# Optimization experiments

Hardware: AMD Instinct MI355X
Metric: run time of the kernel (lower is better)

The kernel has to match this reference:

```python
import jax, jax.numpy as jnp
import numpy as np
import math

B, S, HID = 4, 2048, 2048
H, KV, D = 16, 4, 128  # heads, kv heads, head_dim; n_rep = H//KV = 4
THETA = 1000000.0


def setup_inputs() -> dict:
    key = jax.random.key(0)
    ks = jax.random.split(key, 6)
    x = jax.random.normal(ks[0], (B, S, HID), dtype=jnp.float32)
    # real RoPE tables (theta=1e6), shape [S, D]
    inv_freq = 1.0 / (THETA ** (jnp.arange(0, D, 2, dtype=jnp.float32) / D))
    t = jnp.arange(S, dtype=jnp.float32)
    freqs = jnp.outer(t, inv_freq)                      # [S, D/2]
    emb = jnp.concatenate([freqs, freqs], axis=-1)      # [S, D]
    cos, sin = jnp.cos(emb), jnp.sin(emb)
    scale = 0.02
    wq = jax.random.normal(ks[1], (H * D, HID), dtype=jnp.float32) * scale
    wk = jax.random.normal(ks[2], (KV * D, HID), dtype=jnp.float32) * scale
    wv = jax.random.normal(ks[3], (KV * D, HID), dtype=jnp.float32) * scale
    wo = jax.random.normal(ks[4], (HID, H * D), dtype=jnp.float32) * scale
    return {"x": x, "cos": cos, "sin": sin, "wq": wq, "wk": wk, "wv": wv, "wo": wo}


def _rotate_half(t):
    half = t.shape[-1] // 2
    return jnp.concatenate([-t[..., half:], t[..., :half]], axis=-1)


def reference(x, cos, sin, wq, wk, wv, wo):
    b, s, _ = x.shape
    rep = H // KV
    # QKV projections (torch Linear: y = x @ W^T)
    q = (x @ wq.T).reshape(b, s, H, D)
    k = (x @ wk.T).reshape(b, s, KV, D)
    v = (x @ wv.T).reshape(b, s, KV, D)
    # RoPE, cos/sin broadcast over batch and heads: [1, S, 1, D]
    c = cos[None, :s, None, :]
    si = sin[None, :s, None, :]
    q = q * c + _rotate_half(q) * si
    k = k * c + _rotate_half(k) * si
    # GQA without materializing repeated KV: group q heads as [KV, rep]
    qg = q.reshape(b, s, KV, rep, D)
    scale = 1.0 / math.sqrt(D)
    # flash path in source: SDPA with default is_causal=False -> full (non-causal) attention
    scores = jnp.einsum('bqkrd,bskd->bkrqs', qg, k) * scale  # [B, KV, rep, S, S]
    attn = jax.nn.softmax(scores, axis=-1)
    out = jnp.einsum('bkrqs,bskd->bqkrd', attn, v).reshape(b, s, H * D)
    return out @ wo.T
```

## Files before the change

kernel.cpp:

```cpp
#include <hip/hip_runtime.h>
#include <stdint.h>

#define BB 4
#define SS 2048
#define HIDW 2048
#define NH 16
#define NKV 4
#define DD 128

typedef unsigned short u16;
typedef unsigned long long u64;
typedef unsigned int uint;
typedef __attribute__((ext_vector_type(8))) short bf16x8;
typedef __attribute__((ext_vector_type(4))) float f32x4;
typedef __attribute__((ext_vector_type(2))) float f32x2;
typedef __attribute__((ext_vector_type(2))) __bf16 bf16x2;

__device__ __forceinline__ u16 f2bf1(float f) {
  __bf16 h = (__bf16)f;
  return __builtin_bit_cast(u16, h);
}

__device__ __forceinline__ float bf2f(u16 v) {
  return __uint_as_float((uint)v << 16);
}

__device__ __forceinline__ uint pkbf(float a, float b) {
  f32x2 v = {a, b};
  bf16x2 h = __builtin_convertvector(v, bf16x2);
  return __builtin_bit_cast(uint, h);
}

__device__ __forceinline__ void gld_lds16(const void* g, void* s) {
  __builtin_amdgcn_global_load_lds(
      (const __attribute__((address_space(1))) void*)g,
      (__attribute__((address_space(3))) void*)(unsigned)(uintptr_t)s,
      16, 0, 0);
}

__global__ __launch_bounds__(256) void cast_f32_bf16(const float* __restrict__ in,
                                                     u16* __restrict__ out, int n4) {
  int i = blockIdx.x * 256 + threadIdx.x;
  if (i < n4) {
    float4 f = ((const float4*)in)[i];
    uint2 o;
    o.x = pkbf(f.x, f.y);
    o.y = pkbf(f.z, f.w);
    ((uint2*)out)[i] = o;
  }
}

__global__ __launch_bounds__(256) void gemm_bt(const u16* __restrict__ A,
                                               const u16* __restrict__ Bt,
                                               float* __restrict__ C,
                                               int M, int N, int K) {
  __shared__ u16 As[128 * 32];
  __shared__ u16 Bs[128 * 32];
  const int tid = threadIdx.x;
  const int wave = tid >> 6, lane = tid & 63;
  const int lr = lane & 15, lq = lane >> 4;
  const int row0 = blockIdx.y * 128, col0 = blockIdx.x * 128;
  const int wm = (wave >> 1) * 64, wn = (wave & 1) * 64;

  const int trow = tid >> 2;
  const int tblk = (tid & 3) ^ (trow & 3);
  const u16* aSrc = A + (size_t)(row0 + trow) * K + tblk * 8;
  const u16* bSrc = Bt + (size_t)(col0 + trow) * K + tblk * 8;
  char* ldsA = (char*)As + wave * 1024;
  char* ldsB = (char*)Bs + wave * 1024;

  f32x4 acc[4][4] = {};
  const int aoff = (wm + lr) * 32 + ((lq ^ (lr & 3)) * 8);
  const int boff = (wn + lr) * 32 + ((lq ^ (lr & 3)) * 8);

  for (int k0 = 0; k0 < K; k0 += 32) {
    __syncthreads();
    gld_lds16(aSrc + k0, ldsA);
    gld_lds16(aSrc + (size_t)64 * K + k0, ldsA + 4096);
    gld_lds16(bSrc + k0, ldsB);
    gld_lds16(bSrc + (size_t)64 * K + k0, ldsB + 4096);
    __syncthreads();
    bf16x8 a[4], b[4];
#pragma unroll
    for (int i = 0; i < 4; i++) a[i] = *(const bf16x8*)(As + aoff + i * 512);
#pragma unroll
    for (int j = 0; j < 4; j++) b[j] = *(const bf16x8*)(Bs + boff + j * 512);
#pragma unroll
    for (int i = 0; i < 4; i++)
#pragma unroll
      for (int j = 0; j < 4; j++)
        acc[i][j] = __builtin_amdgcn_mfma_f32_16x16x32_bf16(a[i], b[j], acc[i][j], 0, 0, 0);
  }
#pragma unroll
  for (int i = 0; i < 4; i++) {
    int row = row0 + wm + i * 16 + lq * 4;
#pragma unroll
    for (int j = 0; j < 4; j++) {
      int col = col0 + wn + j * 16 + lr;
      float* cp = C + (size_t)row * N + col;
#pragma unroll
      for (int r = 0; r < 4; r++) cp[(size_t)r * N] = acc[i][j][r];
    }
  }
}

__global__ __launch_bounds__(256) void gemm_bt_bf16(const u16* __restrict__ A,
                                                    const u16* __restrict__ Bt,
                                                    u16* __restrict__ C,
                                                    int M, int N, int K) {
  __shared__ u16 As[128 * 32];
  __shared__ u16 Bs[128 * 32];
  const int tid = threadIdx.x;
  const int wave = tid >> 6, lane = tid & 63;
  const int lr = lane & 15, lq = lane >> 4;
  const int row0 = blockIdx.y * 128, col0 = blockIdx.x * 128;
  const int wm = (wave >> 1) * 64, wn = (wave & 1) * 64;

  const int trow = tid >> 2;
  const int tblk = (tid & 3) ^ (trow & 3);
  const u16* aSrc = A + (size_t)(row0 + trow) * K + tblk * 8;
  const u16* bSrc = Bt + (size_t)(col0 + trow) * K + tblk * 8;
  char* ldsA = (char*)As + wave * 1024;
  char* ldsB = (char*)Bs + wave * 1024;

  f32x4 acc[4][4] = {};
  const int aoff = (wm + lr) * 32 + ((lq ^ (lr & 3)) * 8);
  const int boff = (wn + lr) * 32 + ((lq ^ (lr & 3)) * 8);

  for (int k0 = 0; k0 < K; k0 += 32) {
    __syncthreads();
    gld_lds16(aSrc + k0, ldsA);
    gld_lds16(aSrc + (size_t)64 * K + k0, ldsA + 4096);
    gld_lds16(bSrc + k0, ldsB);
    gld_lds16(bSrc + (size_t)64 * K + k0, ldsB + 4096);
    __syncthreads();
    bf16x8 a[4], b[4];
#pragma unroll
    for (int i = 0; i < 4; i++) a[i] = *(const bf16x8*)(As + aoff + i * 512);
#pragma unroll
    for (int j = 0; j < 4; j++) b[j] = *(const bf16x8*)(Bs + boff + j * 512);
#pragma unroll
    for (int i = 0; i < 4; i++)
#pragma unroll
      for (int j = 0; j < 4; j++)
        acc[i][j] = __builtin_amdgcn_mfma_f32_16x16x32_bf16(a[i], b[j], acc[i][j], 0, 0, 0);
  }
#pragma unroll
  for (int i = 0; i < 4; i++) {
    int row = row0 + wm + i * 16 + lq * 4;
#pragma unroll
    for (int j = 0; j < 4; j++) {
      int col = col0 + wn + j * 16 + lr;
      u16* cp = C + (size_t)row * N + col;
#pragma unroll
      for (int r = 0; r < 4; r++) cp[(size_t)r * N] = f2bf1(acc[i][j][r]);
    }
  }
}

__global__ __launch_bounds__(256) void rope_qk(const u16* __restrict__ qkv,
                                               const float* __restrict__ cosT,
                                               const float* __restrict__ sinT,
                                               u16* __restrict__ qb, u16* __restrict__ kb) {
  const float qscale = 0.08838834764831845f;
  int tok = blockIdx.x;
  int b = tok >> 11, s = tok & (SS - 1);
  for (int p = threadIdx.x; p < (NH + NKV) * 64; p += 256) {
    int head = p >> 6, dd = p & 63;
    float c0 = cosT[s * DD + dd];
    float c1 = cosT[s * DD + dd + 64];
    float s0 = sinT[s * DD + dd];
    float s1 = sinT[s * DD + dd + 64];
    if (head < NH) {
      const u16* src = qkv + (size_t)tok * 3072 + head * DD;
      float x0 = bf2f(src[dd]), x1 = bf2f(src[dd + 64]);
      u16* dst = qb + ((size_t)(b * NH + head) * SS + s) * DD;
      dst[dd] = f2bf1((x0 * c0 - x1 * s0) * qscale);
      dst[dd + 64] = f2bf1((x1 * c1 + x0 * s1) * qscale);
    } else {
      int kv = head - NH;
      const u16* src = qkv + (size_t)tok * 3072 + 2048 + kv * DD;
      float x0 = bf2f(src[dd]), x1 = bf2f(src[dd + 64]);
      u16* dst = kb + ((size_t)(b * NKV + kv) * SS + s) * DD;
      dst[dd] = f2bf1(x0 * c0 - x1 * s0);
      dst[dd + 64] = f2bf1(x1 * c1 + x0 * s1);
    }
  }
}

__global__ __launch_bounds__(256) void v_trans(const u16* __restrict__ qkv,
                                               u16* __restrict__ vt) {
  __shared__ u16 tile[64][66];
  int bk = blockIdx.x;
  int b = bk >> 2, kv = bk & 3;
  int s0 = blockIdx.y * 64, d0 = blockIdx.z * 64;
  int t = threadIdx.x;
  int sl = t >> 2, dc = (t & 3) * 16;
  const u16* src = qkv + ((size_t)(b * SS + s0 + sl)) * 3072 + 2560 + kv * DD + d0 + dc;
  uint4 a0 = *(const uint4*)src;
  uint4 a1 = *(const uint4*)(src + 8);
  uint* lrow = (uint*)&tile[sl][dc];
  lrow[0] = a0.x; lrow[1] = a0.y; lrow[2] = a0.z; lrow[3] = a0.w;
  lrow[4] = a1.x; lrow[5] = a1.y; lrow[6] = a1.z; lrow[7] = a1.w;
  __syncthreads();
  int dl = t >> 2, sc = (t & 3) * 16;
  u16* dst = vt + ((size_t)bk * DD + d0 + dl) * SS + s0 + sc;
  uint4 o0, o1;
  o0.x = (uint)tile[sc + 0][dl] | ((uint)tile[sc + 1][dl] << 16);
  o0.y = (uint)tile[sc + 2][dl] | ((uint)tile[sc + 3][dl] << 16);
  o0.z = (uint)tile[sc + 4][dl] | ((uint)tile[sc + 5][dl] << 16);
  o0.w = (uint)tile[sc + 6][dl] | ((uint)tile[sc + 7][dl] << 16);
  o1.x = (uint)tile[sc + 8][dl] | ((uint)tile[sc + 9][dl] << 16);
  o1.y = (uint)tile[sc + 10][dl] | ((uint)tile[sc + 11][dl] << 16);
  o1.z = (uint)tile[sc + 12][dl] | ((uint)tile[sc + 13][dl] << 16);
  o1.w = (uint)tile[sc + 14][dl] | ((uint)tile[sc + 15][dl] << 16);
  *(uint4*)dst = o0;
  *(uint4*)(dst + 8) = o1;
}

__global__ __launch_bounds__(256, 2) void flash_attn(const u16* __restrict__ qb,
                                                     const u16* __restrict__ kb,
                                                     const u16* __restrict__ vt,
                                                     u16* __restrict__ ob) {
  __shared__ u16 Ks[2][64 * 128];
  __shared__ u16 Vs[2][128 * 64];
  __shared__ u16 Pt[128 * 64];
  const int tid = threadIdx.x;
  const int wave = tid >> 6, lane = tid & 63;
  const int lr = lane & 15, lq = lane >> 4;

  const int lin = blockIdx.y * 16 + blockIdx.x;
  const int xcd = lin & 7;
  const int slot = lin >> 3;
  const int pr = xcd + ((slot & 1) << 3);
  const int b = pr >> 2, kvh = pr & 3;
  const int rest = slot >> 1;
  const int h = kvh * 4 + (rest & 3);
  const int q0 = (rest >> 2) * 128;
  const int bh = b * 16 + h;

  const size_t kbase = (size_t)(b * NKV + kvh) * SS * DD;
  const size_t vbase = (size_t)(b * NKV + kvh) * DD * SS;

  bf16x8 qf[2][4];
#pragma unroll
  for (int nt = 0; nt < 2; nt++) {
    const u16* qrow = qb + ((size_t)bh * SS + q0 + wave * 32 + nt * 16 + lr) * DD + lq * 8;
#pragma unroll
    for (int kk = 0; kk < 4; kk++) qf[nt][kk] = *(const bf16x8*)(qrow + kk * 32);
  }

  f32x4 o_acc[8][2] = {};
  float l_i[2] = {0.0f, 0.0f};

  const int ktrow = tid >> 4;
  const int ktblk = (tid & 15) ^ ktrow;
  const u16* ksrc = kb + kbase + (size_t)ktrow * DD + ktblk * 8;
  const int vtrow = tid >> 3;
  const int vtblk = (tid & 7) ^ (vtrow & 7);
  const u16* vsrc = vt + vbase + (size_t)vtrow * SS + vtblk * 8;

  for (int s0 = 0; s0 < SS; s0 += 128) {
    __syncthreads();
#pragma unroll
    for (int hb = 0; hb < 2; hb++) {
      const u16* kS = ksrc + (size_t)(s0 + hb * 64) * DD;
      const u16* vS = vsrc + s0 + hb * 64;
      char* kd = (char*)(Ks[hb]) + wave * 1024;
      char* vd = (char*)(Vs[hb]) + wave * 1024;
#pragma unroll
      for (int c = 0; c < 4; c++) {
        gld_lds16(kS + (size_t)c * 16 * DD, kd + c * 4096);
        gld_lds16(vS + (size_t)c * 32 * SS, vd + c * 4096);
      }
    }
    __syncthreads();

#pragma unroll
    for (int hb = 0; hb < 2; hb++) {
      const u16* K = Ks[hb];
      const u16* V = Vs[hb];

      f32x4 sc[4][2] = {};
#pragma unroll
      for (int kk = 0; kk < 4; kk++) {
#pragma unroll
        for (int mt = 0; mt < 4; mt++) {
          bf16x8 kf = *(const bf16x8*)(K + (mt * 16 + lr) * 128 + (((kk * 4 + lq) ^ lr) * 8));
#pragma unroll
          for (int nt = 0; nt < 2; nt++)
            sc[mt][nt] = __builtin_amdgcn_mfma_f32_16x16x32_bf16(kf, qf[nt][kk], sc[mt][nt], 0, 0, 0);
        }
      }

#pragma unroll
      for (int nt = 0; nt < 2; nt++) {
        float rs = 0.0f;
#pragma unroll
        for (int mt = 0; mt < 4; mt++)
#pragma unroll
          for (int r = 0; r < 4; r++) {
            float p = __expf(sc[mt][nt][r]);
            sc[mt][nt][r] = p;
            rs += p;
          }
        l_i[nt] += rs;
        int prow = wave * 32 + nt * 16 + lr;
#pragma unroll
        for (int mt = 0; mt < 4; mt++) {
          u64 pw = (u64)pkbf(sc[mt][nt][0], sc[mt][nt][1]) |
                   ((u64)pkbf(sc[mt][nt][2], sc[mt][nt][3]) << 32);
          int bb = (mt * 2 + (lq >> 1)) ^ (lr & 7);
          *(u64*)((char*)Pt + prow * 128 + bb * 16 + (lq & 1) * 8) = pw;
        }
      }

#pragma unroll
      for (int kk2 = 0; kk2 < 2; kk2++) {
        bf16x8 pbf[2];
#pragma unroll
        for (int nt = 0; nt < 2; nt++) {
          int prow = wave * 32 + nt * 16 + lr;
          pbf[nt] = *(const bf16x8*)((char*)Pt + prow * 128 + (((kk2 * 4 + lq) ^ (lr & 7)) * 16));
        }
#pragma unroll
        for (int mt = 0; mt < 8; mt++) {
          bf16x8 vf = *(const bf16x8*)(V + (mt * 16 + lr) * 64 + (((kk2 * 4 + lq) ^ (lr & 7)) * 8));
#pragma unroll
          for (int nt = 0; nt < 2; nt++)
            o_acc[mt][nt] = __builtin_amdgcn_mfma_f32_16x16x32_bf16(vf, pbf[nt], o_acc[mt][nt], 0, 0, 0);
        }
      }
    }
  }

#pragma unroll
  for (int nt = 0; nt < 2; nt++) {
    float l = l_i[nt];
    l += __shfl_xor(l, 16, 64);
    l += __shfl_xor(l, 32, 64);
    float inv = 1.0f / l;
    size_t q = (size_t)q0 + wave * 32 + nt * 16 + lr;
    u16* dst = ob + ((size_t)b * SS + q) * HIDW + h * DD + lq * 4;
#pragma unroll
    for (int mt = 0; mt < 8; mt++) {
      uint2 pk;
      pk.x = pkbf(o_acc[mt][nt][0] * inv, o_acc[mt][nt][1] * inv);
      pk.y = pkbf(o_acc[mt][nt][2] * inv, o_acc[mt][nt][3] * inv);
      *(uint2*)(dst + mt * 16) = pk;
    }
  }
}

extern "C" void kernel_launch(void* const* d_in, const int* in_sizes, int n_in,
                              void* d_out, int out_size, void* d_ws, size_t ws_size,
                              hipStream_t stream) {
  const float* x = (const float*)d_in[0];
  const float* cosT = (const float*)d_in[1];
  const float* sinT = (const float*)d_in[2];
  const float* wq = (const float*)d_in[3];
  const float* wk = (const float*)d_in[4];
  const float* wv = (const float*)d_in[5];
  const float* wo = (const float*)d_in[6];
  float* out = (float*)d_out;

  char* ws = (char*)d_ws;
  size_t off = 0;
  auto alloc = [&](size_t bytes) {
    char* p = ws + off;
    off += (bytes + 255) & ~(size_t)255;
    return p;
  };
  const int M = BB * SS;
  u16* xb = (u16*)alloc((size_t)M * HIDW * 2);
  u16* wqkvb = (u16*)alloc((size_t)3072 * HIDW * 2);
  u16* wob = (u16*)alloc((size_t)HIDW * NH * DD * 2);
  u16* qkvb = (u16*)alloc((size_t)M * 3072 * 2);
  u16* qb = (u16*)alloc((size_t)BB * NH * SS * DD * 2);
  u16* kb = (u16*)alloc((size_t)BB * NKV * SS * DD * 2);
  u16* vt = (u16*)alloc((size_t)BB * NKV * DD * SS * 2);
  u16* ob = qkvb;

  cast_f32_bf16<<<(M * HIDW) / 1024, 256, 0, stream>>>(x, xb, (M * HIDW) / 4);
  cast_f32_bf16<<<(2048 * HIDW) / 1024, 256, 0, stream>>>(wq, wqkvb, (2048 * HIDW) / 4);
  cast_f32_bf16<<<(512 * HIDW) / 1024, 256, 0, stream>>>(wk, wqkvb + (size_t)2048 * HIDW,
                                                         (512 * HIDW) / 4);
  cast_f32_bf16<<<(512 * HIDW) / 1024, 256, 0, stream>>>(wv, wqkvb + (size_t)2560 * HIDW,
                                                         (512 * HIDW) / 4);
  cast_f32_bf16<<<(HIDW * NH * DD) / 1024, 256, 0, stream>>>(wo, wob, (HIDW * NH * DD) / 4);

  gemm_bt_bf16<<<dim3(3072 / 128, M / 128), 256, 0, stream>>>(xb, wqkvb, qkvb, M, 3072, HIDW);

  rope_qk<<<M, 256, 0, stream>>>(qkvb, cosT, sinT, qb, kb);
  v_trans<<<dim3(BB * NKV, SS / 64, DD / 64), 256, 0, stream>>>(qkvb, vt);

  flash_attn<<<dim3(SS / 128, BB * NH), 256, 0, stream>>>(qb, kb, vt, ob);

  gemm_bt<<<dim3(HIDW / 128, M / 128), 256, 0, stream>>>(ob, wob, out, M, HIDW, NH * DD);
}
```

Before: 554.3 us.

## Fuse RoPE and V transpose into QKV GEMM epilogue, merge weight casts

The QKV projection GEMM changes its warp tiling so each wave holds 32 rows by a full 128-column head. The epilogue can then apply RoPE and the q scale, or write V transposed, directly from the accumulators. This removes the intermediate qkv buffer round-trip and the separate rope_qk and v_trans kernels. The four weight cast launches are merged into one kernel. The cost is epilogue stores that are less coalesced, per-element cos/sin loads in the GEMM, and a different MFMA operand load pattern.

```diff
diff --git a/kernel.cpp b/kernel.cpp
--- a/kernel.cpp
+++ b/kernel.cpp
@@ -48,6 +48,32 @@
     o.y = pkbf(f.z, f.w);
     ((uint2*)out)[i] = o;
   }
+}
+
+__global__ __launch_bounds__(256) void cast_weights(const float* __restrict__ wq,
+                                                    const float* __restrict__ wk,
+                                                    const float* __restrict__ wv,
+                                                    const float* __restrict__ wo,
+                                                    u16* __restrict__ wqkvb,
+                                                    u16* __restrict__ wob) {
+  int i = blockIdx.x * 256 + threadIdx.x;
+  const float* src;
+  uint2* dst;
+  int off;
+  if (i < 1048576) {
+    src = wq; dst = (uint2*)wqkvb; off = i;
+  } else if (i < 1310720) {
+    src = wk; dst = (uint2*)(wqkvb + (size_t)2048 * 2048); off = i - 1048576;
+  } else if (i < 1572864) {
+    src = wv; dst = (uint2*)(wqkvb + (size_t)2560 * 2048); off = i - 1310720;
+  } else {
+    src = wo; dst = (uint2*)wob; off = i - 1572864;
+  }
+  float4 f = ((const float4*)src)[off];
+  uint2 o;
+  o.x = pkbf(f.x, f.y);
+  o.y = pkbf(f.z, f.w);
+  dst[off] = o;
 }
 
 __global__ __launch_bounds__(256) void gemm_bt(const u16* __restrict__ A,
@@ -104,17 +130,20 @@
   }
 }
 
-__global__ __launch_bounds__(256) void gemm_bt_bf16(const u16* __restrict__ A,
-                                                    const u16* __restrict__ Bt,
-                                                    u16* __restrict__ C,
-                                                    int M, int N, int K) {
+__global__ __launch_bounds__(256) void gemm_qkv_rope(const u16* __restrict__ A,
+                                                     const u16* __restrict__ Bt,
+                                                     const float* __restrict__ cosT,
+                                                     const float* __restrict__ sinT,
+                                                     u16* __restrict__ qb,
+                                                     u16* __restrict__ kb,
+                                                     u16* __restrict__ vt) {
   __shared__ u16 As[128 * 32];
   __shared__ u16 Bs[128 * 32];
   const int tid = threadIdx.x;
   const int wave = tid >> 6, lane = tid & 63;
   const int lr = lane & 15, lq = lane >> 4;
   const int row0 = blockIdx.y * 128, col0 = blockIdx.x * 128;
-  const int wm = (wave >> 1) * 64, wn = (wave & 1) * 64;
+  const int K = HIDW;
 
   const int trow = tid >> 2;
   const int tblk = (tid & 3) ^ (trow & 3);
@@ -123,9 +152,9 @@
   char* ldsA = (char*)As + wave * 1024;
   char* ldsB = (char*)Bs + wave * 1024;
 
-  f32x4 acc[4][4] = {};
-  const int aoff = (wm + lr) * 32 + ((lq ^ (lr & 3)) * 8);
-  const int boff = (wn + lr) * 32 + ((lq ^ (lr & 3)) * 8);
+  f32x4 acc[2][8] = {};
+  const int aoff = (wave * 32 + lr) * 32 + ((lq ^ (lr & 3)) * 8);
+  const int boff = lr * 32 + ((lq ^ (lr & 3)) * 8);
 
   for (int k0 = 0; k0 < K; k0 += 32) {
     __syncthreads();
@@ -134,88 +163,59 @@
     gld_lds16(bSrc + k0, ldsB);
     gld_lds16(bSrc + (size_t)64 * K + k0, ldsB + 4096);
     __syncthreads();
-    bf16x8 a[4], b[4];
-#pragma unroll
-    for (int i = 0; i < 4; i++) a[i] = *(const bf16x8*)(As + aoff + i * 512);
-#pragma unroll
-    for (int j = 0; j < 4; j++) b[j] = *(const bf16x8*)(Bs + boff + j * 512);
-#pragma unroll
-    for (int i = 0; i < 4; i++)
-#pragma unroll
-      for (int j = 0; j < 4; j++)
+    bf16x8 a[2], b[8];
+#pragma unroll
+    for (int i = 0; i < 2; i++) a[i] = *(const bf16x8*)(As + aoff + i * 512);
+#pragma unroll
+    for (int j = 0; j < 8; j++) b[j] = *(const bf16x8*)(Bs + boff + j * 512);
+#pragma unroll
+    for (int i = 0; i < 2; i++)
+#pragma unroll
+      for (int j = 0; j < 8; j++)
         acc[i][j] = __builtin_amdgcn_mfma_f32_16x16x32_bf16(a[i], b[j], acc[i][j], 0, 0, 0);
   }
-#pragma unroll
-  for (int i = 0; i < 4; i++) {
-    int row = row0 + wm + i * 16 + lq * 4;
-#pragma unroll
-    for (int j = 0; j < 4; j++) {
-      int col = col0 + wn + j * 16 + lr;
-      u16* cp = C + (size_t)row * N + col;
-#pragma unroll
-      for (int r = 0; r < 4; r++) cp[(size_t)r * N] = f2bf1(acc[i][j][r]);
-    }
-  }
-}
-
-__global__ __launch_bounds__(256) void rope_qk(const u16* __restrict__ qkv,
-                                               const float* __restrict__ cosT,
-                                               const float* __restrict__ sinT,
-                                               u16* __restrict__ qb, u16* __restrict__ kb) {
-  const float qscale = 0.08838834764831845f;
-  int tok = blockIdx.x;
-  int b = tok >> 11, s = tok & (SS - 1);
-  for (int p = threadIdx.x; p < (NH + NKV) * 64; p += 256) {
-    int head = p >> 6, dd = p & 63;
-    float c0 = cosT[s * DD + dd];
-    float c1 = cosT[s * DD + dd + 64];
-    float s0 = sinT[s * DD + dd];
-    float s1 = sinT[s * DD + dd + 64];
-    if (head < NH) {
-      const u16* src = qkv + (size_t)tok * 3072 + head * DD;
-      float x0 = bf2f(src[dd]), x1 = bf2f(src[dd + 64]);
-      u16* dst = qb + ((size_t)(b * NH + head) * SS + s) * DD;
-      dst[dd] = f2bf1((x0 * c0 - x1 * s0) * qscale);
-      dst[dd + 64] = f2bf1((x1 * c1 + x0 * s1) * qscale);
-    } else {
-      int kv = head - NH;
-      const u16* src = qkv + (size_t)tok * 3072 + 2048 + kv * DD;
-      float x0 = bf2f(src[dd]), x1 = bf2f(src[dd + 64]);
-      u16* dst = kb + ((size_t)(b * NKV + kv) * SS + s) * DD;
-      dst[dd] = f2bf1(x0 * c0 - x1 * s0);
-      dst[dd + 64] = f2bf1(x1 * c1 + x0 * s1);
-    }
-  }
-}
-
-__global__ __launch_bounds__(256) void v_trans(const u16* __restrict__ qkv,
-                                               u16* __restrict__ vt) {
-  __shared__ u16 tile[64][66];
-  int bk = blockIdx.x;
-  int b = bk >> 2, kv = bk & 3;
-  int s0 = blockIdx.y * 64, d0 = blockIdx.z * 64;
-  int t = threadIdx.x;
-  int sl = t >> 2, dc = (t & 3) * 16;
-  const u16* src = qkv + ((size_t)(b * SS + s0 + sl)) * 3072 + 2560 + kv * DD + d0 + dc;
-  uint4 a0 = *(const uint4*)src;
-  uint4 a1 = *(const uint4*)(src + 8);
-  uint* lrow = (uint*)&tile[sl][dc];
-  lrow[0] = a0.x; lrow[1] = a0.y; lrow[2] = a0.z; lrow[3] = a0.w;
-  lrow[4] = a1.x; lrow[5] = a1.y; lrow[6] = a1.z; lrow[7] = a1.w;
-  __syncthreads();
-  int dl = t >> 2, sc = (t & 3) * 16;
-  u16* dst = vt + ((size_t)bk * DD + d0 + dl) * SS + s0 + sc;
-  uint4 o0, o1;
-  o0.x = (uint)tile[sc + 0][dl] | ((uint)tile[sc + 1][dl] << 16);
-  o0.y = (uint)tile[sc + 2][dl] | ((uint)tile[sc + 3][dl] << 16);
-  o0.z = (uint)tile[sc + 4][dl] | ((uint)tile[sc + 5][dl] << 16);
-  o0.w = (uint)tile[sc + 6][dl] | ((uint)tile[sc + 7][dl] << 16);
-  o1.x = (uint)tile[sc + 8][dl] | ((uint)tile[sc + 9][dl] << 16);
-  o1.y = (uint)tile[sc + 10][dl] | ((uint)tile[sc + 11][dl] << 16);
-  o1.z = (uint)tile[sc + 12][dl] | ((uint)tile[sc + 13][dl] << 16);
-  o1.w = (uint)tile[sc + 14][dl] | ((uint)tile[sc + 15][dl] << 16);
-  *(uint4*)dst = o0;
-  *(uint4*)(dst + 8) = o1;
+
+  const int b_ = row0 >> 11;
+  const int s_base = (row0 & (SS - 1)) + wave * 32;
+  const int hsel = col0 >> 7;
+
+  if (hsel < 20) {
+    const float scale = (hsel < 16) ? 0.08838834764831845f : 1.0f;
+    u16* base = (hsel < 16)
+                    ? qb + (size_t)(b_ * NH + hsel) * SS * DD
+                    : kb + (size_t)(b_ * NKV + (hsel - 16)) * SS * DD;
+#pragma unroll
+    for (int i = 0; i < 2; i++) {
+#pragma unroll
+      for (int r = 0; r < 4; r++) {
+        int s = s_base + i * 16 + lq * 4 + r;
+        const float* cp = cosT + (size_t)s * DD;
+        const float* sp = sinT + (size_t)s * DD;
+        u16* drow = base + (size_t)s * DD;
+#pragma unroll
+        for (int j = 0; j < 4; j++) {
+          int d = j * 16 + lr;
+          float c = cp[d], si = sp[d];
+          float x0 = acc[i][j][r] * scale, x1 = acc[i][j + 4][r] * scale;
+          drow[d] = f2bf1(x0 * c - x1 * si);
+          drow[d + 64] = f2bf1(x1 * c + x0 * si);
+        }
+      }
+    }
+  } else {
+    const int kv = hsel - 20;
+#pragma unroll
+    for (int i = 0; i < 2; i++) {
+      int s = s_base + i * 16 + lq * 4;
+#pragma unroll
+      for (int j = 0; j < 8; j++) {
+        int d = j * 16 + lr;
+        u64 pw = (u64)pkbf(acc[i][j][0], acc[i][j][1]) |
+                 ((u64)pkbf(acc[i][j][2], acc[i][j][3]) << 32);
+        *(u64*)(vt + (size_t)((b_ * NKV + kv) * DD + d) * SS + s) = pw;
+      }
+    }
+  }
 }
 
 __global__ __launch_bounds__(256, 2) void flash_attn(const u16* __restrict__ qb,
@@ -375,24 +375,16 @@
   u16* xb = (u16*)alloc((size_t)M * HIDW * 2);
   u16* wqkvb = (u16*)alloc((size_t)3072 * HIDW * 2);
   u16* wob = (u16*)alloc((size_t)HIDW * NH * DD * 2);
-  u16* qkvb = (u16*)alloc((size_t)M * 3072 * 2);
   u16* qb = (u16*)alloc((size_t)BB * NH * SS * DD * 2);
   u16* kb = (u16*)alloc((size_t)BB * NKV * SS * DD * 2);
   u16* vt = (u16*)alloc((size_t)BB * NKV * DD * SS * 2);
-  u16* ob = qkvb;
+  u16* ob = (u16*)alloc((size_t)M * HIDW * 2);
 
   cast_f32_bf16<<<(M * HIDW) / 1024, 256, 0, stream>>>(x, xb, (M * HIDW) / 4);
-  cast_f32_bf16<<<(2048 * HIDW) / 1024, 256, 0, stream>>>(wq, wqkvb, (2048 * HIDW) / 4);
-  cast_f32_bf16<<<(512 * HIDW) / 1024, 256, 0, stream>>>(wk, wqkvb + (size_t)2048 * HIDW,
-                                                         (512 * HIDW) / 4);
-  cast_f32_bf16<<<(512 * HIDW) / 1024, 256, 0, stream>>>(wv, wqkvb + (size_t)2560 * HIDW,
-                                                         (512 * HIDW) / 4);
-  cast_f32_bf16<<<(HIDW * NH * DD) / 1024, 256, 0, stream>>>(wo, wob, (HIDW * NH * DD) / 4);
-
-  gemm_bt_bf16<<<dim3(3072 / 128, M / 128), 256, 0, stream>>>(xb, wqkvb, qkvb, M, 3072, HIDW);
-
-  rope_qk<<<M, 256, 0, stream>>>(qkvb, cosT, sinT, qb, kb);
-  v_trans<<<dim3(BB * NKV, SS / 64, DD / 64), 256, 0, stream>>>(qkvb, vt);
+  cast_weights<<<10240, 256, 0, stream>>>(wq, wk, wv, wo, wqkvb, wob);
+
+  gemm_qkv_rope<<<dim3(3072 / 128, M / 128), 256, 0, stream>>>(xb, wqkvb, cosT, sinT,
+                                                               qb, kb, vt);
 
   flash_attn<<<dim3(SS / 128, BB * NH), 256, 0, stream>>>(qb, kb, vt, ob);
 
```

Result: faster. 535.2 us (-3.4%).
